# Kernel optimization log

Measured on AMD Instinct MI355X. Metric: run time of the kernel, lower is better.

The kernel has to match this reference:

```python
import jax, jax.numpy as jnp
import numpy as np

N, E, H, ED = 20000, 640000, 128, 16


def _lin_init(k, fan_in, fan_out):
    kw, kb = jax.random.split(k)
    lim = 1.0 / np.sqrt(fan_in)
    W = jax.random.uniform(kw, (fan_in, fan_out), jnp.float32, -lim, lim)
    b = jax.random.uniform(kb, (fan_out,), jnp.float32, -lim, lim)
    return W, b


def setup_inputs() -> dict:
    key = jax.random.key(0)
    ks = jax.random.split(key, 12)
    h = jax.random.normal(ks[0], (N, H), jnp.float32)
    x = jax.random.normal(ks[1], (N, 3), jnp.float32)
    edge_index = jax.random.randint(ks[2], (2, E), 0, N, jnp.int32)
    edge_attr = jax.random.normal(ks[3], (E, ED), jnp.float32)
    fixed_mask = jax.random.randint(ks[4], (N,), 0, 2, jnp.int32).astype(bool)
    We1, be1 = _lin_init(ks[5], 2 * H + 1 + ED, H)
    We2, be2 = _lin_init(ks[6], H, H)
    Wx1, bx1 = _lin_init(ks[7], H, H)
    Wx2, bx2 = _lin_init(ks[8], H, 1)
    Wh1, bh1 = _lin_init(ks[9], 2 * H, H)
    Wh2, bh2 = _lin_init(ks[10], H, H)
    return {"h": h, "x": x, "edge_index": edge_index, "edge_attr": edge_attr,
            "fixed_mask": fixed_mask,
            "We1": We1, "be1": be1, "We2": We2, "be2": be2,
            "Wx1": Wx1, "bx1": bx1, "Wx2": Wx2, "bx2": bx2,
            "Wh1": Wh1, "bh1": bh1, "Wh2": Wh2, "bh2": bh2}


def reference(h, x, edge_index, edge_attr, fixed_mask,
              We1, be1, We2, be2, Wx1, bx1, Wx2, bx2, Wh1, bh1, Wh2, bh2):
    src, dst = edge_index[0], edge_index[1]
    n = h.shape[0]
    diff = x[src] - x[dst]                               # [E,3]
    dist_sq_norm = jnp.sum(diff * diff, -1, keepdims=True) / 100.0
    e_in = jnp.concatenate([h[src], h[dst], dist_sq_norm, edge_attr], -1)
    m_ij = jax.nn.silu(jax.nn.silu(e_in @ We1 + be1) @ We2 + be2)  # [E,H]
    coord_w = jnp.tanh(jax.nn.silu(m_ij @ Wx1 + bx1) @ Wx2 + bx2)  # [E,1]
    coord_agg = jax.ops.segment_sum(diff * coord_w, dst, num_segments=n)
    coord_agg = coord_agg * (~fixed_mask).astype(h.dtype)[:, None]
    msg_agg = jax.ops.segment_sum(m_ij, dst, num_segments=n)       # [N,H]
    h_new = h + jax.nn.silu(jnp.concatenate([h, msg_agg], -1) @ Wh1 + bh1) @ Wh2 + bh2
    x_new = x + coord_agg
    return h_new, x_new
```

## Files before the change

### kernel.cpp

```cpp
#include <hip/hip_runtime.h>
#include <hip/hip_bf16.h>
#include <math.h>

#define NN   20000
#define NE   640000
#define HD   128
#define EDIM 16
#define KIN  273
#define P2   136

#define S_PWT   4096
#define S_PWE1M 32768
#define S_PW4   16384
#define S_PWH1  32768
#define S_PWH2  16384

typedef __bf16 bf16x8 __attribute__((ext_vector_type(8)));
typedef float  f32x4  __attribute__((ext_vector_type(4)));

__device__ __forceinline__ float silu_f(float v) {
    const float e = __expf(-v);
    return v * __builtin_amdgcn_rcpf(1.0f + e);
}
__device__ __forceinline__ float tanh_f(float s) {
    const float e = __expf(2.0f * s);
    return 1.0f - 2.0f * __builtin_amdgcn_rcpf(e + 1.0f);
}
__device__ __forceinline__ unsigned short f2bf(float f) {
    __bf16 b = (__bf16)f;
    return __builtin_bit_cast(unsigned short, b);
}
__device__ __forceinline__ float bf2f(unsigned short u) {
    __bf16 b = __builtin_bit_cast(__bf16, u);
    return (float)b;
}
__device__ __forceinline__ unsigned pack2bf(float a, float b) {
    return (unsigned)f2bf(a) | ((unsigned)f2bf(b) << 16);
}

__device__ __forceinline__ void pack_id(const float* __restrict__ W, int Kreal,
                                        unsigned short* __restrict__ P, int idx) {
    const int f = idx >> 9, r = idx & 511;
    const int lane = r >> 3, j = r & 7;
    const int kb = f >> 3, nb = f & 7;
    const int k = kb * 32 + (lane >> 4) * 8 + j;
    const int n = nb * 16 + (lane & 15);
    P[idx] = f2bf((k < Kreal) ? W[(size_t)k * HD + n] : 0.0f);
}
__device__ __forceinline__ void pack_il(const float* __restrict__ W, int Kreal,
                                        unsigned short* __restrict__ P, int idx) {
    const int f = idx >> 9, r = idx & 511;
    const int lane = r >> 3, j = r & 7;
    const int kb = f >> 3, nb = f & 7;
    const int k = kb * 32 + (lane >> 4) * 8 + j;
    const int n = (nb >> 1) * 32 + 2 * (lane & 15) + (nb & 1);
    P[idx] = f2bf((k < Kreal) ? W[(size_t)k * HD + n] : 0.0f);
}

__global__ void egnn_prep_kernel(
    const float* __restrict__ h, const int* __restrict__ ei,
    const float* __restrict__ We1, const float* __restrict__ We2,
    const float* __restrict__ Wx1, const float* __restrict__ Wh1,
    const float* __restrict__ Wh2,
    unsigned short* __restrict__ hb,
    unsigned short* __restrict__ PWt,  unsigned short* __restrict__ PWe1m,
    unsigned short* __restrict__ PWe2, unsigned short* __restrict__ PWx1,
    unsigned short* __restrict__ PWh1, unsigned short* __restrict__ PWh2,
    int* __restrict__ cnt)
{
    const size_t NH = (size_t)NN * HD;
    const size_t T1 = NH + S_PWT, T2 = T1 + S_PWE1M, T3 = T2 + S_PW4;
    const size_t T4 = T3 + S_PW4, T5 = T4 + S_PWH1, T6 = T5 + S_PWH2;
    const size_t TOT = T6 + NE;
    const size_t stride = (size_t)gridDim.x * blockDim.x;
    for (size_t i = (size_t)blockIdx.x * blockDim.x + threadIdx.x; i < TOT; i += stride) {
        if (i < NH) { hb[i] = f2bf(h[i]); continue; }
        if (i < T1) {
            const int idx = (int)(i - NH);
            const int r = idx & 511, nb = idx >> 9;
            const int lane = r >> 3, j = r & 7;
            const int k = 256 + (lane >> 4) * 8 + j;
            const int n = (nb >> 1) * 32 + 2 * (lane & 15) + (nb & 1);
            PWt[idx] = f2bf((k < KIN) ? We1[(size_t)k * HD + n] : 0.0f);
            continue;
        }
        if (i < T2) { pack_il(We1, 256, PWe1m, (int)(i - T1)); continue; }
        if (i < T3) { pack_il(We2, HD, PWe2, (int)(i - T2)); continue; }
        if (i < T4) { pack_il(Wx1, HD, PWx1, (int)(i - T3)); continue; }
        if (i < T5) { pack_id(Wh1, 2 * HD, PWh1, (int)(i - T4)); continue; }
        if (i < T6) { pack_id(Wh2, HD, PWh2, (int)(i - T5)); continue; }
        atomicAdd(&cnt[ei[NE + (i - T6)]], 1);
    }
}

__global__ __launch_bounds__(256, 4) void egnn_pre_kernel(
    const unsigned short* __restrict__ hb,
    const unsigned short* __restrict__ PWe1m, const float* __restrict__ be1,
    const int* __restrict__ cnt, int* __restrict__ cursor,
    unsigned short* __restrict__ preS, unsigned short* __restrict__ preD)
{
    const int t = threadIdx.x;
    if (blockIdx.x == 313) {
        __shared__ int ls[256];
        const int base = t * 79;
        int c[79];
        int s = 0;
        for (int i = 0; i < 79; ++i) {
            const int idx = base + i;
            c[i] = (idx < NN) ? cnt[idx] : 0;
            s += c[i];
        }
        ls[t] = s;
        __syncthreads();
        int v = s;
        for (int off = 1; off < 256; off <<= 1) {
            const int u = (t >= off) ? ls[t - off] : 0;
            __syncthreads();
            v += u;
            ls[t] = v;
            __syncthreads();
        }
        int run = v - s;
        for (int i = 0; i < 79; ++i) {
            const int idx = base + i;
            if (idx < NN) { cursor[idx] = run; run += c[i]; }
        }
        return;
    }
    const int n0 = blockIdx.x * 64;
    const int lane = t & 63, w = t >> 6;
    const int quad = lane >> 4, l16 = lane & 15;
    int arow[4];
    #pragma unroll
    for (int mb = 0; mb < 4; ++mb) arow[mb] = min(n0 + mb * 16 + l16, NN - 1);

    f32x4 accS[4][2], accD[4][2];
    #pragma unroll
    for (int mb = 0; mb < 4; ++mb)
        #pragma unroll
        for (int nt = 0; nt < 2; ++nt) {
            accS[mb][nt] = (f32x4){0.f,0.f,0.f,0.f};
            accD[mb][nt] = (f32x4){0.f,0.f,0.f,0.f};
        }
    #pragma unroll
    for (int kb = 0; kb < 4; ++kb) {
        bf16x8 a[4], bS[2], bD[2];
        #pragma unroll
        for (int mb = 0; mb < 4; ++mb)
            a[mb] = *(const bf16x8*)&hb[(size_t)arow[mb] * HD + kb * 32 + quad * 8];
        #pragma unroll
        for (int nt = 0; nt < 2; ++nt) {
            bS[nt] = *(const bf16x8*)&PWe1m[((kb * 8 + w * 2 + nt) * 64 + lane) * 8];
            bD[nt] = *(const bf16x8*)&PWe1m[(((4 + kb) * 8 + w * 2 + nt) * 64 + lane) * 8];
        }
        #pragma unroll
        for (int mb = 0; mb < 4; ++mb)
            #pragma unroll
            for (int nt = 0; nt < 2; ++nt) {
                accS[mb][nt] = __builtin_amdgcn_mfma_f32_16x16x32_bf16(
                    a[mb], bS[nt], accS[mb][nt], 0, 0, 0);
                accD[mb][nt] = __builtin_amdgcn_mfma_f32_16x16x32_bf16(
                    a[mb], bD[nt], accD[mb][nt], 0, 0, 0);
            }
    }
    const int cb = w * 32 + 2 * l16;
    const float2 b1 = *(const float2*)&be1[cb];
    #pragma unroll
    for (int mb = 0; mb < 4; ++mb)
        #pragma unroll
        for (int r = 0; r < 4; ++r) {
            const int n = n0 + mb * 16 + quad * 4 + r;
            if (n < NN) {
                *(unsigned*)&preS[(size_t)n * HD + cb] =
                    pack2bf(accS[mb][0][r], accS[mb][1][r]);
                *(unsigned*)&preD[(size_t)n * HD + cb] =
                    pack2bf(accD[mb][0][r] + b1.x, accD[mb][1][r] + b1.y);
            }
        }
}

__global__ void egnn_perm_kernel(const int* __restrict__ ei,
                                 int* __restrict__ cursor, int* __restrict__ perm) {
    const int e = blockIdx.x * 256 + threadIdx.x;
    const int pos = atomicAdd(&cursor[ei[NE + e]], 1);
    perm[pos] = e;
}

__global__ __launch_bounds__(256, 4) void egnn_edge_kernel(
    const unsigned short* __restrict__ preS, const unsigned short* __restrict__ preD,
    const float* __restrict__ x,
    const int* __restrict__ ei, const float* __restrict__ eattr,
    const int* __restrict__ perm,
    const unsigned short* __restrict__ PWt,
    const unsigned short* __restrict__ PWe2, const float* __restrict__ be2,
    const unsigned short* __restrict__ PWx1, const float* __restrict__ bx1,
    const float* __restrict__ Wx2, const float* __restrict__ bx2,
    float* __restrict__ msg_agg, float* __restrict__ coord_agg)
{
    __shared__ __align__(16) unsigned short tail[64 * 32];
    __shared__ __align__(16) unsigned short sT[64 * P2];
    __shared__ __align__(16) unsigned short sM[64 * P2];
    __shared__ int   sE[64], sSrc[64], sDst[64];
    __shared__ float sDiff[64][3];
    __shared__ float sW[64];

    const int t  = threadIdx.x;
    const int e0 = blockIdx.x * 64;

    if (t < 64) {
        const int e = perm[e0 + t];
        sE[t] = e;
        const int s = ei[e];
        const int d = ei[NE + e];
        sSrc[t] = s; sDst[t] = d;
        const float dx = x[s*3+0] - x[d*3+0];
        const float dy = x[s*3+1] - x[d*3+1];
        const float dz = x[s*3+2] - x[d*3+2];
        sDiff[t][0] = dx; sDiff[t][1] = dy; sDiff[t][2] = dz;
        tail[t * 32 + 0] = f2bf((dx*dx + dy*dy + dz*dz) * 0.01f);
    }
    __syncthreads();

    const int lane = t & 63;
    const int w    = t >> 6;
    const int quad = lane >> 4;
    const int l16  = lane & 15;
    const int cb   = w * 32 + 2 * l16;

    f32x4 preC[4][2];
    #pragma unroll
    for (int mb = 0; mb < 4; ++mb)
        #pragma unroll
        for (int r = 0; r < 4; ++r) {
            const int row = mb * 16 + quad * 4 + r;
            const unsigned us = *(const unsigned*)&preS[(size_t)sSrc[row] * HD + cb];
            const unsigned ud = *(const unsigned*)&preD[(size_t)sDst[row] * HD + cb];
            preC[mb][0][r] = bf2f((unsigned short)(us & 0xffff)) +
                             bf2f((unsigned short)(ud & 0xffff));
            preC[mb][1][r] = bf2f((unsigned short)(us >> 16)) +
                             bf2f((unsigned short)(ud >> 16));
        }

    {
        const int eL = t >> 2, q = t & 3;
        const int eG = sE[eL];
        #pragma unroll
        for (int jj = 0; jj < 8; ++jj) {
            const int col = q * 8 + jj;
            if (col == 0) continue;
            float v = 0.0f;
            if (col <= EDIM) v = eattr[(size_t)eG * EDIM + (col - 1)];
            tail[eL * 32 + col] = f2bf(v);
        }
    }
    __syncthreads();

    f32x4 acc1[4][2];
    {
        bf16x8 a[4], b[2];
        #pragma unroll
        for (int mb = 0; mb < 4; ++mb)
            a[mb] = *(const bf16x8*)&tail[(mb * 16 + l16) * 32 + quad * 8];
        #pragma unroll
        for (int nt = 0; nt < 2; ++nt)
            b[nt] = *(const bf16x8*)&PWt[((w * 2 + nt) * 64 + lane) * 8];
        #pragma unroll
        for (int mb = 0; mb < 4; ++mb)
            #pragma unroll
            for (int nt = 0; nt < 2; ++nt)
                acc1[mb][nt] = __builtin_amdgcn_mfma_f32_16x16x32_bf16(
                    a[mb], b[nt], preC[mb][nt], 0, 0, 0);
    }
    #pragma unroll
    for (int mb = 0; mb < 4; ++mb)
        #pragma unroll
        for (int r = 0; r < 4; ++r) {
            const int row = mb * 16 + quad * 4 + r;
            *(unsigned*)&sT[row * P2 + cb] =
                pack2bf(silu_f(acc1[mb][0][r]), silu_f(acc1[mb][1][r]));
        }
    __syncthreads();

    f32x4 acc2[4][2];
    #pragma unroll
    for (int mb = 0; mb < 4; ++mb)
        #pragma unroll
        for (int nt = 0; nt < 2; ++nt) acc2[mb][nt] = (f32x4){0.f,0.f,0.f,0.f};
    #pragma unroll
    for (int kb = 0; kb < 4; ++kb) {
        bf16x8 a[4], b[2];
        #pragma unroll
        for (int mb = 0; mb < 4; ++mb)
            a[mb] = *(const bf16x8*)&sT[(mb * 16 + l16) * P2 + kb * 32 + quad * 8];
        #pragma unroll
        for (int nt = 0; nt < 2; ++nt)
            b[nt] = *(const bf16x8*)&PWe2[((kb * 8 + w * 2 + nt) * 64 + lane) * 8];
        #pragma unroll
        for (int mb = 0; mb < 4; ++mb)
            #pragma unroll
            for (int nt = 0; nt < 2; ++nt)
                acc2[mb][nt] = __builtin_amdgcn_mfma_f32_16x16x32_bf16(
                    a[mb], b[nt], acc2[mb][nt], 0, 0, 0);
    }
    {
        const float2 b2 = *(const float2*)&be2[cb];
        #pragma unroll
        for (int mb = 0; mb < 4; ++mb)
            #pragma unroll
            for (int r = 0; r < 4; ++r) {
                const int row = mb * 16 + quad * 4 + r;
                *(unsigned*)&sM[row * P2 + cb] =
                    pack2bf(silu_f(acc2[mb][0][r] + b2.x),
                            silu_f(acc2[mb][1][r] + b2.y));
            }
    }
    __syncthreads();

    {
        const int ch   = t & 127;
        const int half = t >> 7;
        const int r0   = half * 32;
        float acc = 0.0f;
        #pragma unroll 4
        for (int r = 0; r < 32; ++r) {
            const int row = r0 + r;
            const int d   = sDst[row];
            acc += bf2f(sM[row * P2 + ch]);
            const bool flush = (r == 31) || (sDst[row + 1] != d);
            if (flush) {
                atomicAdd(&msg_agg[(size_t)d * HD + ch], acc);
                acc = 0.0f;
            }
        }
    }

    f32x4 acc3[4][2];
    #pragma unroll
    for (int mb = 0; mb < 4; ++mb)
        #pragma unroll
        for (int nt = 0; nt < 2; ++nt) acc3[mb][nt] = (f32x4){0.f,0.f,0.f,0.f};
    #pragma unroll
    for (int kb = 0; kb < 4; ++kb) {
        bf16x8 a[4], b[2];
        #pragma unroll
        for (int mb = 0; mb < 4; ++mb)
            a[mb] = *(const bf16x8*)&sM[(mb * 16 + l16) * P2 + kb * 32 + quad * 8];
        #pragma unroll
        for (int nt = 0; nt < 2; ++nt)
            b[nt] = *(const bf16x8*)&PWx1[((kb * 8 + w * 2 + nt) * 64 + lane) * 8];
        #pragma unroll
        for (int mb = 0; mb < 4; ++mb)
            #pragma unroll
            for (int nt = 0; nt < 2; ++nt)
                acc3[mb][nt] = __builtin_amdgcn_mfma_f32_16x16x32_bf16(
                    a[mb], b[nt], acc3[mb][nt], 0, 0, 0);
    }
    {
        const float2 bx = *(const float2*)&bx1[cb];
        const float2 w2 = *(const float2*)&Wx2[cb];
        float p[4][4];
        #pragma unroll
        for (int mb = 0; mb < 4; ++mb)
            #pragma unroll
            for (int r = 0; r < 4; ++r)
                p[mb][r] = silu_f(acc3[mb][0][r] + bx.x) * w2.x +
                           silu_f(acc3[mb][1][r] + bx.y) * w2.y;
        #pragma unroll
        for (int off = 8; off >= 1; off >>= 1)
            #pragma unroll
            for (int mb = 0; mb < 4; ++mb)
                #pragma unroll
                for (int r = 0; r < 4; ++r)
                    p[mb][r] += __shfl_xor(p[mb][r], off, 64);
        if (l16 == 0) {
            float* red = reinterpret_cast<float*>(sT);
            #pragma unroll
            for (int mb = 0; mb < 4; ++mb)
                #pragma unroll
                for (int r = 0; r < 4; ++r)
                    red[w * 64 + mb * 16 + quad * 4 + r] = p[mb][r];
        }
    }
    __syncthreads();
    if (t < 64) {
        const float* red = reinterpret_cast<const float*>(sT);
        sW[t] = tanh_f(red[t] + red[64 + t] + red[128 + t] + red[192 + t] + bx2[0]);
    }
    __syncthreads();

    if (w < 3) {
        const int dstv = sDst[lane];
        float v = sDiff[lane][w] * sW[lane];
        #pragma unroll
        for (int off = 1; off <= 32; off <<= 1) {
            const int   dn = __shfl_down(dstv, off, 64);
            const float vn = __shfl_down(v, off, 64);
            if (lane + off < 64 && dn == dstv) v += vn;
        }
        const int up = __shfl_up(dstv, 1, 64);
        if (lane == 0 || up != dstv)
            atomicAdd(&coord_agg[(size_t)dstv * 3 + w], v);
    }
}

__global__ __launch_bounds__(256, 4) void egnn_node_kernel(
    const unsigned short* __restrict__ hb, const float* __restrict__ h,
    const float* __restrict__ x, const int* __restrict__ fixed_mask,
    const unsigned short* __restrict__ PWh1, const float* __restrict__ bh1,
    const unsigned short* __restrict__ PWh2, const float* __restrict__ bh2,
    const float* __restrict__ msg_agg, const float* __restrict__ coord_agg,
    float* __restrict__ out_h, float* __restrict__ out_x)
{
    __shared__ __align__(16) unsigned short sTn[64 * P2];
    const int t  = threadIdx.x;
    const int n0 = blockIdx.x * 64;
    const int lane = t & 63, w = t >> 6;
    const int quad = lane >> 4, l16 = lane & 15;

    if (t < 192) {
        const int ln = t / 3, d3 = t - ln * 3;
        const int n  = n0 + ln;
        if (n < NN) {
            const float add = (fixed_mask[n] != 0) ? 0.0f : coord_agg[(size_t)n*3 + d3];
            out_x[(size_t)n*3 + d3] = x[(size_t)n*3 + d3] + add;
        }
    }

    int nrow[4];
    #pragma unroll
    for (int mb = 0; mb < 4; ++mb) nrow[mb] = min(n0 + mb * 16 + l16, NN - 1);

    f32x4 acc[4][2];
    #pragma unroll
    for (int mb = 0; mb < 4; ++mb)
        #pragma unroll
        for (int nt = 0; nt < 2; ++nt) acc[mb][nt] = (f32x4){0.f,0.f,0.f,0.f};

    #pragma unroll
    for (int kb = 0; kb < 8; ++kb) {
        bf16x8 a[4], b[2];
        if (kb < 4) {
            #pragma unroll
            for (int mb = 0; mb < 4; ++mb)
                a[mb] = *(const bf16x8*)&hb[(size_t)nrow[mb] * HD + kb * 32 + quad * 8];
        } else {
            #pragma unroll
            for (int mb = 0; mb < 4; ++mb) {
                const float* mp = msg_agg + (size_t)nrow[mb] * HD + (kb - 4) * 32 + quad * 8;
                const float4 v0 = ((const float4*)mp)[0];
                const float4 v1 = ((const float4*)mp)[1];
                bf16x8 av;
                av[0]=(__bf16)v0.x; av[1]=(__bf16)v0.y; av[2]=(__bf16)v0.z; av[3]=(__bf16)v0.w;
                av[4]=(__bf16)v1.x; av[5]=(__bf16)v1.y; av[6]=(__bf16)v1.z; av[7]=(__bf16)v1.w;
                a[mb] = av;
            }
        }
        #pragma unroll
        for (int nt = 0; nt < 2; ++nt)
            b[nt] = *(const bf16x8*)&PWh1[((kb * 8 + w * 2 + nt) * 64 + lane) * 8];
        #pragma unroll
        for (int mb = 0; mb < 4; ++mb)
            #pragma unroll
            for (int nt = 0; nt < 2; ++nt)
                acc[mb][nt] = __builtin_amdgcn_mfma_f32_16x16x32_bf16(
                    a[mb], b[nt], acc[mb][nt], 0, 0, 0);
    }
    #pragma unroll
    for (int nt = 0; nt < 2; ++nt) {
        const int col = w * 32 + nt * 16 + l16;
        const float bias = bh1[col];
        #pragma unroll
        for (int mb = 0; mb < 4; ++mb)
            #pragma unroll
            for (int r = 0; r < 4; ++r) {
                const int row = mb * 16 + quad * 4 + r;
                sTn[row * P2 + col] = f2bf(silu_f(acc[mb][nt][r] + bias));
            }
    }
    __syncthreads();

    #pragma unroll
    for (int mb = 0; mb < 4; ++mb)
        #pragma unroll
        for (int nt = 0; nt < 2; ++nt) acc[mb][nt] = (f32x4){0.f,0.f,0.f,0.f};
    #pragma unroll
    for (int kb = 0; kb < 4; ++kb) {
        bf16x8 a[4], b[2];
        #pragma unroll
        for (int mb = 0; mb < 4; ++mb)
            a[mb] = *(const bf16x8*)&sTn[(mb * 16 + l16) * P2 + kb * 32 + quad * 8];
        #pragma unroll
        for (int nt = 0; nt < 2; ++nt)
            b[nt] = *(const bf16x8*)&PWh2[((kb * 8 + w * 2 + nt) * 64 + lane) * 8];
        #pragma unroll
        for (int mb = 0; mb < 4; ++mb)
            #pragma unroll
            for (int nt = 0; nt < 2; ++nt)
                acc[mb][nt] = __builtin_amdgcn_mfma_f32_16x16x32_bf16(
                    a[mb], b[nt], acc[mb][nt], 0, 0, 0);
    }
    #pragma unroll
    for (int nt = 0; nt < 2; ++nt) {
        const int col = w * 32 + nt * 16 + l16;
        const float bias = bh2[col];
        #pragma unroll
        for (int mb = 0; mb < 4; ++mb)
            #pragma unroll
            for (int r = 0; r < 4; ++r) {
                const int row = mb * 16 + quad * 4 + r;
                const int n   = n0 + row;
                if (n < NN)
                    out_h[(size_t)n * HD + col] =
                        h[(size_t)n * HD + col] + acc[mb][nt][r] + bias;
            }
    }
}

extern "C" void kernel_launch(void* const* d_in, const int* in_sizes, int n_in,
                              void* d_out, int out_size, void* d_ws, size_t ws_size,
                              hipStream_t stream)
{
    const float* h     = (const float*)d_in[0];
    const float* x     = (const float*)d_in[1];
    const int*   ei    = (const int*)d_in[2];
    const float* eattr = (const float*)d_in[3];
    const int*   fmask = (const int*)d_in[4];
    const float* We1   = (const float*)d_in[5];
    const float* be1   = (const float*)d_in[6];
    const float* We2   = (const float*)d_in[7];
    const float* be2   = (const float*)d_in[8];
    const float* Wx1   = (const float*)d_in[9];
    const float* bx1   = (const float*)d_in[10];
    const float* Wx2   = (const float*)d_in[11];
    const float* bx2   = (const float*)d_in[12];
    const float* Wh1   = (const float*)d_in[13];
    const float* bh1   = (const float*)d_in[14];
    const float* Wh2   = (const float*)d_in[15];
    const float* bh2   = (const float*)d_in[16];

    float* msg    = (float*)d_ws;
    float* coord  = msg + (size_t)NN * HD;
    int*   cnt    = (int*)(coord + (size_t)NN * 3);
    int*   cursor = cnt + NN;
    int*   perm   = cursor + NN;
    unsigned short* hb    = (unsigned short*)(perm + NE);
    unsigned short* preS  = hb + (size_t)NN * HD;
    unsigned short* preD  = preS + (size_t)NN * HD;
    unsigned short* PWt   = preD + (size_t)NN * HD;
    unsigned short* PWe1m = PWt + S_PWT;
    unsigned short* PWe2  = PWe1m + S_PWE1M;
    unsigned short* PWx1  = PWe2 + S_PW4;
    unsigned short* PWh1  = PWx1 + S_PW4;
    unsigned short* PWh2  = PWh1 + S_PWH1;

    float* out_h = (float*)d_out;
    float* out_x = out_h + (size_t)NN * HD;

    hipMemsetAsync(d_ws, 0, (size_t)NN * (HD + 3 + 1) * sizeof(float), stream);
    egnn_prep_kernel<<<1024, 256, 0, stream>>>(
        h, ei, We1, We2, Wx1, Wh1, Wh2,
        hb, PWt, PWe1m, PWe2, PWx1, PWh1, PWh2, cnt);
    egnn_pre_kernel<<<314, 256, 0, stream>>>(hb, PWe1m, be1, cnt, cursor, preS, preD);
    egnn_perm_kernel<<<NE / 256, 256, 0, stream>>>(ei, cursor, perm);
    egnn_edge_kernel<<<NE / 64, 256, 0, stream>>>(
        preS, preD, x, ei, eattr, perm, PWt, PWe2, be2, PWx1, bx1,
        Wx2, bx2, msg, coord);
    egnn_node_kernel<<<(NN + 63) / 64, 256, 0, stream>>>(
        hb, h, x, fmask, PWh1, bh1, PWh2, bh2, msg, coord, out_h, out_x);
}
```

Before: 396.4 us.

## Merge memset, prep, pre-GEMM and permutation build into one cooperative kernel

```diff
diff --git a/kernel.cpp b/kernel.cpp
--- a/kernel.cpp
+++ b/kernel.cpp
@@ -1,6 +1,9 @@
 #include <hip/hip_runtime.h>
 #include <hip/hip_bf16.h>
+#include <hip/hip_cooperative_groups.h>
 #include <math.h>
+
+namespace cg = cooperative_groups;
 
 #define NN   20000
 #define NE   640000
@@ -14,6 +17,11 @@
 #define S_PW4   16384
 #define S_PWH1  32768
 #define S_PWH2  16384
+#define WPACK   (S_PWT + S_PWE1M + 2*S_PW4 + S_PWH1 + S_PWH2)
+
+#define COOPB   512
+#define ZDW     (NN*HD + NN*3 + NN)
+#define HCAST4  (NN*HD/4)
 
 typedef __bf16 bf16x8 __attribute__((ext_vector_type(8)));
 typedef float  f32x4  __attribute__((ext_vector_type(4)));
@@ -57,57 +65,127 @@
     P[idx] = f2bf((k < Kreal) ? W[(size_t)k * HD + n] : 0.0f);
 }
 
-__global__ void egnn_prep_kernel(
+__global__ __launch_bounds__(256, 2) void egnn_coop_kernel(
     const float* __restrict__ h, const int* __restrict__ ei,
     const float* __restrict__ We1, const float* __restrict__ We2,
     const float* __restrict__ Wx1, const float* __restrict__ Wh1,
-    const float* __restrict__ Wh2,
+    const float* __restrict__ Wh2, const float* __restrict__ be1,
+    int* __restrict__ zbase,
     unsigned short* __restrict__ hb,
     unsigned short* __restrict__ PWt,  unsigned short* __restrict__ PWe1m,
     unsigned short* __restrict__ PWe2, unsigned short* __restrict__ PWx1,
     unsigned short* __restrict__ PWh1, unsigned short* __restrict__ PWh2,
-    int* __restrict__ cnt)
+    unsigned short* __restrict__ preS, unsigned short* __restrict__ preD,
+    int* __restrict__ cnt, int* __restrict__ cursor, int* __restrict__ perm)
 {
-    const size_t NH = (size_t)NN * HD;
-    const size_t T1 = NH + S_PWT, T2 = T1 + S_PWE1M, T3 = T2 + S_PW4;
-    const size_t T4 = T3 + S_PW4, T5 = T4 + S_PWH1, T6 = T5 + S_PWH2;
-    const size_t TOT = T6 + NE;
-    const size_t stride = (size_t)gridDim.x * blockDim.x;
-    for (size_t i = (size_t)blockIdx.x * blockDim.x + threadIdx.x; i < TOT; i += stride) {
-        if (i < NH) { hb[i] = f2bf(h[i]); continue; }
-        if (i < T1) {
-            const int idx = (int)(i - NH);
-            const int r = idx & 511, nb = idx >> 9;
-            const int lane = r >> 3, j = r & 7;
-            const int k = 256 + (lane >> 4) * 8 + j;
-            const int n = (nb >> 1) * 32 + 2 * (lane & 15) + (nb & 1);
-            PWt[idx] = f2bf((k < KIN) ? We1[(size_t)k * HD + n] : 0.0f);
-            continue;
-        }
-        if (i < T2) { pack_il(We1, 256, PWe1m, (int)(i - T1)); continue; }
-        if (i < T3) { pack_il(We2, HD, PWe2, (int)(i - T2)); continue; }
-        if (i < T4) { pack_il(Wx1, HD, PWx1, (int)(i - T3)); continue; }
-        if (i < T5) { pack_id(Wh1, 2 * HD, PWh1, (int)(i - T4)); continue; }
-        if (i < T6) { pack_id(Wh2, HD, PWh2, (int)(i - T5)); continue; }
-        atomicAdd(&cnt[ei[NE + (i - T6)]], 1);
-    }
-}
-
-__global__ __launch_bounds__(256, 4) void egnn_pre_kernel(
-    const unsigned short* __restrict__ hb,
-    const unsigned short* __restrict__ PWe1m, const float* __restrict__ be1,
-    const int* __restrict__ cnt, int* __restrict__ cursor,
-    unsigned short* __restrict__ preS, unsigned short* __restrict__ preD)
-{
+    cg::grid_group grid = cg::this_grid();
     const int t = threadIdx.x;
-    if (blockIdx.x == 313) {
+    const int b = blockIdx.x;
+    const int gid = b * 256 + t;
+    const int gstride = COOPB * 256;
+
+    {
+        const int TOT = ZDW + HCAST4 + WPACK;
+        for (int i = gid; i < TOT; i += gstride) {
+            if (i < ZDW) { zbase[i] = 0; continue; }
+            int r = i - ZDW;
+            if (r < HCAST4) {
+                const float4 v = ((const float4*)h)[r];
+                unsigned* dst = (unsigned*)&hb[(size_t)r * 4];
+                dst[0] = pack2bf(v.x, v.y);
+                dst[1] = pack2bf(v.z, v.w);
+                continue;
+            }
+            r -= HCAST4;
+            if (r < S_PWT) {
+                const int rr = r & 511, nb = r >> 9;
+                const int lane = rr >> 3, j = rr & 7;
+                const int k = 256 + (lane >> 4) * 8 + j;
+                const int n = (nb >> 1) * 32 + 2 * (lane & 15) + (nb & 1);
+                PWt[r] = f2bf((k < KIN) ? We1[(size_t)k * HD + n] : 0.0f);
+                continue;
+            }
+            r -= S_PWT;
+            if (r < S_PWE1M) { pack_il(We1, 256, PWe1m, r); continue; }
+            r -= S_PWE1M;
+            if (r < S_PW4) { pack_il(We2, HD, PWe2, r); continue; }
+            r -= S_PW4;
+            if (r < S_PW4) { pack_il(Wx1, HD, PWx1, r); continue; }
+            r -= S_PW4;
+            if (r < S_PWH1) { pack_id(Wh1, 2 * HD, PWh1, r); continue; }
+            r -= S_PWH1;
+            pack_id(Wh2, HD, PWh2, r);
+        }
+    }
+    grid.sync();
+
+    if (b < 313) {
+        const int n0 = b * 64;
+        const int lane = t & 63, w = t >> 6;
+        const int quad = lane >> 4, l16 = lane & 15;
+        int arow[4];
+        #pragma unroll
+        for (int mb = 0; mb < 4; ++mb) arow[mb] = min(n0 + mb * 16 + l16, NN - 1);
+
+        f32x4 accS[4][2], accD[4][2];
+        #pragma unroll
+        for (int mb = 0; mb < 4; ++mb)
+            #pragma unroll
+            for (int nt = 0; nt < 2; ++nt) {
+                accS[mb][nt] = (f32x4){0.f,0.f,0.f,0.f};
+                accD[mb][nt] = (f32x4){0.f,0.f,0.f,0.f};
+            }
+        #pragma unroll
+        for (int kb = 0; kb < 4; ++kb) {
+            bf16x8 a[4], bS[2], bD[2];
+            #pragma unroll
+            for (int mb = 0; mb < 4; ++mb)
+                a[mb] = *(const bf16x8*)&hb[(size_t)arow[mb] * HD + kb * 32 + quad * 8];
+            #pragma unroll
+            for (int nt = 0; nt < 2; ++nt) {
+                bS[nt] = *(const bf16x8*)&PWe1m[((kb * 8 + w * 2 + nt) * 64 + lane) * 8];
+                bD[nt] = *(const bf16x8*)&PWe1m[(((4 + kb) * 8 + w * 2 + nt) * 64 + lane) * 8];
+            }
+            #pragma unroll
+            for (int mb = 0; mb < 4; ++mb)
+                #pragma unroll
+                for (int nt = 0; nt < 2; ++nt) {
+                    accS[mb][nt] = __builtin_amdgcn_mfma_f32_16x16x32_bf16(
+                        a[mb], bS[nt], accS[mb][nt], 0, 0, 0);
+                    accD[mb][nt] = __builtin_amdgcn_mfma_f32_16x16x32_bf16(
+                        a[mb], bD[nt], accD[mb][nt], 0, 0, 0);
+                }
+        }
+        const int cb = w * 32 + 2 * l16;
+        const float2 b1 = *(const float2*)&be1[cb];
+        #pragma unroll
+        for (int mb = 0; mb < 4; ++mb)
+            #pragma unroll
+            for (int r = 0; r < 4; ++r) {
+                const int n = n0 + mb * 16 + quad * 4 + r;
+                if (n < NN) {
+                    *(unsigned*)&preS[(size_t)n * HD + cb] =
+                        pack2bf(accS[mb][0][r], accS[mb][1][r]);
+                    *(unsigned*)&preD[(size_t)n * HD + cb] =
+                        pack2bf(accD[mb][0][r] + b1.x, accD[mb][1][r] + b1.y);
+                }
+            }
+    } else {
+        for (int e = (b - 313) * 256 + t; e < NE; e += (COOPB - 313) * 256)
+            atomicAdd(&cnt[ei[NE + e]], 1);
+    }
+    grid.sync();
+
+    if (b == 0) {
         __shared__ int ls[256];
         const int base = t * 79;
         int c[79];
         int s = 0;
         for (int i = 0; i < 79; ++i) {
             const int idx = base + i;
-            c[i] = (idx < NN) ? cnt[idx] : 0;
+            c[i] = (idx < NN)
+                 ? __hip_atomic_load(&cnt[idx], __ATOMIC_RELAXED, __HIP_MEMORY_SCOPE_AGENT)
+                 : 0;
             s += c[i];
         }
         ls[t] = s;
@@ -123,67 +201,19 @@
         int run = v - s;
         for (int i = 0; i < 79; ++i) {
             const int idx = base + i;
-            if (idx < NN) { cursor[idx] = run; run += c[i]; }
-        }
-        return;
-    }
-    const int n0 = blockIdx.x * 64;
-    const int lane = t & 63, w = t >> 6;
-    const int quad = lane >> 4, l16 = lane & 15;
-    int arow[4];
-    #pragma unroll
-    for (int mb = 0; mb < 4; ++mb) arow[mb] = min(n0 + mb * 16 + l16, NN - 1);
-
-    f32x4 accS[4][2], accD[4][2];
-    #pragma unroll
-    for (int mb = 0; mb < 4; ++mb)
-        #pragma unroll
-        for (int nt = 0; nt < 2; ++nt) {
-            accS[mb][nt] = (f32x4){0.f,0.f,0.f,0.f};
-            accD[mb][nt] = (f32x4){0.f,0.f,0.f,0.f};
-        }
-    #pragma unroll
-    for (int kb = 0; kb < 4; ++kb) {
-        bf16x8 a[4], bS[2], bD[2];
-        #pragma unroll
-        for (int mb = 0; mb < 4; ++mb)
-            a[mb] = *(const bf16x8*)&hb[(size_t)arow[mb] * HD + kb * 32 + quad * 8];
-        #pragma unroll
-        for (int nt = 0; nt < 2; ++nt) {
-            bS[nt] = *(const bf16x8*)&PWe1m[((kb * 8 + w * 2 + nt) * 64 + lane) * 8];
-            bD[nt] = *(const bf16x8*)&PWe1m[(((4 + kb) * 8 + w * 2 + nt) * 64 + lane) * 8];
-        }
-        #pragma unroll
-        for (int mb = 0; mb < 4; ++mb)
-            #pragma unroll
-            for (int nt = 0; nt < 2; ++nt) {
-                accS[mb][nt] = __builtin_amdgcn_mfma_f32_16x16x32_bf16(
-                    a[mb], bS[nt], accS[mb][nt], 0, 0, 0);
-                accD[mb][nt] = __builtin_amdgcn_mfma_f32_16x16x32_bf16(
-                    a[mb], bD[nt], accD[mb][nt], 0, 0, 0);
-            }
-    }
-    const int cb = w * 32 + 2 * l16;
-    const float2 b1 = *(const float2*)&be1[cb];
-    #pragma unroll
-    for (int mb = 0; mb < 4; ++mb)
-        #pragma unroll
-        for (int r = 0; r < 4; ++r) {
-            const int n = n0 + mb * 16 + quad * 4 + r;
-            if (n < NN) {
-                *(unsigned*)&preS[(size_t)n * HD + cb] =
-                    pack2bf(accS[mb][0][r], accS[mb][1][r]);
-                *(unsigned*)&preD[(size_t)n * HD + cb] =
-                    pack2bf(accD[mb][0][r] + b1.x, accD[mb][1][r] + b1.y);
-            }
-        }
-}
-
-__global__ void egnn_perm_kernel(const int* __restrict__ ei,
-                                 int* __restrict__ cursor, int* __restrict__ perm) {
-    const int e = blockIdx.x * 256 + threadIdx.x;
-    const int pos = atomicAdd(&cursor[ei[NE + e]], 1);
-    perm[pos] = e;
+            if (idx < NN) {
+                __hip_atomic_store(&cursor[idx], run, __ATOMIC_RELAXED,
+                                   __HIP_MEMORY_SCOPE_AGENT);
+                run += c[i];
+            }
+        }
+    }
+    grid.sync();
+
+    for (int e = gid; e < NE; e += gstride) {
+        const int pos = atomicAdd(&cursor[ei[NE + e]], 1);
+        perm[pos] = e;
+    }
 }
 
 __global__ __launch_bounds__(256, 4) void egnn_edge_kernel(
@@ -556,12 +586,16 @@
     float* out_h = (float*)d_out;
     float* out_x = out_h + (size_t)NN * HD;
 
-    hipMemsetAsync(d_ws, 0, (size_t)NN * (HD + 3 + 1) * sizeof(float), stream);
-    egnn_prep_kernel<<<1024, 256, 0, stream>>>(
-        h, ei, We1, We2, Wx1, Wh1, Wh2,
-        hb, PWt, PWe1m, PWe2, PWx1, PWh1, PWh2, cnt);
-    egnn_pre_kernel<<<314, 256, 0, stream>>>(hb, PWe1m, be1, cnt, cursor, preS, preD);
-    egnn_perm_kernel<<<NE / 256, 256, 0, stream>>>(ei, cursor, perm);
+    int* zbase = (int*)d_ws;
+    void* cargs[] = {
+        (void*)&h, (void*)&ei, (void*)&We1, (void*)&We2, (void*)&Wx1,
+        (void*)&Wh1, (void*)&Wh2, (void*)&be1, (void*)&zbase, (void*)&hb,
+        (void*)&PWt, (void*)&PWe1m, (void*)&PWe2, (void*)&PWx1, (void*)&PWh1,
+        (void*)&PWh2, (void*)&preS, (void*)&preD, (void*)&cnt, (void*)&cursor,
+        (void*)&perm
+    };
+    hipLaunchCooperativeKernel((void*)egnn_coop_kernel, dim3(COOPB), dim3(256),
+                               cargs, 0, stream);
     egnn_edge_kernel<<<NE / 64, 256, 0, stream>>>(
         preS, preD, x, ei, eattr, perm, PWt, PWe2, be2, PWx1, bx1,
         Wx2, bx2, msg, coord);
```

After: 596.8 us. +50.6%, slower.

## Fuse perm build into pre kernel via grid flag; vectorize h cast and msg scatter

Applied to the files above, without the earlier changes.

```diff
diff --git a/kernel.cpp b/kernel.cpp
--- a/kernel.cpp
+++ b/kernel.cpp
@@ -14,6 +14,8 @@
 #define S_PW4   16384
 #define S_PWH1  32768
 #define S_PWH2  16384
+
+#define PREB    314
 
 typedef __bf16 bf16x8 __attribute__((ext_vector_type(8)));
 typedef float  f32x4  __attribute__((ext_vector_type(4)));
@@ -68,15 +70,21 @@
     unsigned short* __restrict__ PWh1, unsigned short* __restrict__ PWh2,
     int* __restrict__ cnt)
 {
-    const size_t NH = (size_t)NN * HD;
-    const size_t T1 = NH + S_PWT, T2 = T1 + S_PWE1M, T3 = T2 + S_PW4;
+    const size_t NH4 = (size_t)NN * HD / 4;
+    const size_t T1 = NH4 + S_PWT, T2 = T1 + S_PWE1M, T3 = T2 + S_PW4;
     const size_t T4 = T3 + S_PW4, T5 = T4 + S_PWH1, T6 = T5 + S_PWH2;
     const size_t TOT = T6 + NE;
     const size_t stride = (size_t)gridDim.x * blockDim.x;
     for (size_t i = (size_t)blockIdx.x * blockDim.x + threadIdx.x; i < TOT; i += stride) {
-        if (i < NH) { hb[i] = f2bf(h[i]); continue; }
+        if (i < NH4) {
+            const float4 v = ((const float4*)h)[i];
+            unsigned* dst = (unsigned*)&hb[(size_t)i * 4];
+            dst[0] = pack2bf(v.x, v.y);
+            dst[1] = pack2bf(v.z, v.w);
+            continue;
+        }
         if (i < T1) {
-            const int idx = (int)(i - NH);
+            const int idx = (int)(i - NH4);
             const int r = idx & 511, nb = idx >> 9;
             const int lane = r >> 3, j = r & 7;
             const int k = 256 + (lane >> 4) * 8 + j;
@@ -93,21 +101,26 @@
     }
 }
 
-__global__ __launch_bounds__(256, 4) void egnn_pre_kernel(
-    const unsigned short* __restrict__ hb,
+__global__ __launch_bounds__(256, 4) void egnn_preperm_kernel(
+    const unsigned short* __restrict__ hb, const int* __restrict__ ei,
     const unsigned short* __restrict__ PWe1m, const float* __restrict__ be1,
     const int* __restrict__ cnt, int* __restrict__ cursor,
+    int* __restrict__ flag, int* __restrict__ perm,
     unsigned short* __restrict__ preS, unsigned short* __restrict__ preD)
 {
     const int t = threadIdx.x;
-    if (blockIdx.x == 313) {
+    const int b = blockIdx.x;
+
+    if (b == 313) {
         __shared__ int ls[256];
         const int base = t * 79;
         int c[79];
         int s = 0;
         for (int i = 0; i < 79; ++i) {
             const int idx = base + i;
-            c[i] = (idx < NN) ? cnt[idx] : 0;
+            c[i] = (idx < NN)
+                 ? __hip_atomic_load(&cnt[idx], __ATOMIC_RELAXED, __HIP_MEMORY_SCOPE_AGENT)
+                 : 0;
             s += c[i];
         }
         ls[t] = s;
@@ -123,67 +136,80 @@
         int run = v - s;
         for (int i = 0; i < 79; ++i) {
             const int idx = base + i;
-            if (idx < NN) { cursor[idx] = run; run += c[i]; }
-        }
-        return;
-    }
-    const int n0 = blockIdx.x * 64;
-    const int lane = t & 63, w = t >> 6;
-    const int quad = lane >> 4, l16 = lane & 15;
-    int arow[4];
-    #pragma unroll
-    for (int mb = 0; mb < 4; ++mb) arow[mb] = min(n0 + mb * 16 + l16, NN - 1);
-
-    f32x4 accS[4][2], accD[4][2];
-    #pragma unroll
-    for (int mb = 0; mb < 4; ++mb)
-        #pragma unroll
-        for (int nt = 0; nt < 2; ++nt) {
-            accS[mb][nt] = (f32x4){0.f,0.f,0.f,0.f};
-            accD[mb][nt] = (f32x4){0.f,0.f,0.f,0.f};
-        }
-    #pragma unroll
-    for (int kb = 0; kb < 4; ++kb) {
-        bf16x8 a[4], bS[2], bD[2];
-        #pragma unroll
-        for (int mb = 0; mb < 4; ++mb)
-            a[mb] = *(const bf16x8*)&hb[(size_t)arow[mb] * HD + kb * 32 + quad * 8];
-        #pragma unroll
-        for (int nt = 0; nt < 2; ++nt) {
-            bS[nt] = *(const bf16x8*)&PWe1m[((kb * 8 + w * 2 + nt) * 64 + lane) * 8];
-            bD[nt] = *(const bf16x8*)&PWe1m[(((4 + kb) * 8 + w * 2 + nt) * 64 + lane) * 8];
-        }
+            if (idx < NN) {
+                __hip_atomic_store(&cursor[idx], run, __ATOMIC_RELAXED,
+                                   __HIP_MEMORY_SCOPE_AGENT);
+                run += c[i];
+            }
+        }
+        __syncthreads();
+        __threadfence();
+        if (t == 0)
+            __hip_atomic_store(flag, 1, __ATOMIC_RELEASE, __HIP_MEMORY_SCOPE_AGENT);
+    } else {
+        const int n0 = b * 64;
+        const int lane = t & 63, w = t >> 6;
+        const int quad = lane >> 4, l16 = lane & 15;
+        int arow[4];
+        #pragma unroll
+        for (int mb = 0; mb < 4; ++mb) arow[mb] = min(n0 + mb * 16 + l16, NN - 1);
+
+        f32x4 accS[4][2], accD[4][2];
         #pragma unroll
         for (int mb = 0; mb < 4; ++mb)
             #pragma unroll
             for (int nt = 0; nt < 2; ++nt) {
-                accS[mb][nt] = __builtin_amdgcn_mfma_f32_16x16x32_bf16(
-                    a[mb], bS[nt], accS[mb][nt], 0, 0, 0);
-                accD[mb][nt] = __builtin_amdgcn_mfma_f32_16x16x32_bf16(
-                    a[mb], bD[nt], accD[mb][nt], 0, 0, 0);
-            }
-    }
-    const int cb = w * 32 + 2 * l16;
-    const float2 b1 = *(const float2*)&be1[cb];
-    #pragma unroll
-    for (int mb = 0; mb < 4; ++mb)
-        #pragma unroll
-        for (int r = 0; r < 4; ++r) {
-            const int n = n0 + mb * 16 + quad * 4 + r;
-            if (n < NN) {
-                *(unsigned*)&preS[(size_t)n * HD + cb] =
-                    pack2bf(accS[mb][0][r], accS[mb][1][r]);
-                *(unsigned*)&preD[(size_t)n * HD + cb] =
-                    pack2bf(accD[mb][0][r] + b1.x, accD[mb][1][r] + b1.y);
-            }
-        }
-}
-
-__global__ void egnn_perm_kernel(const int* __restrict__ ei,
-                                 int* __restrict__ cursor, int* __restrict__ perm) {
-    const int e = blockIdx.x * 256 + threadIdx.x;
-    const int pos = atomicAdd(&cursor[ei[NE + e]], 1);
-    perm[pos] = e;
+                accS[mb][nt] = (f32x4){0.f,0.f,0.f,0.f};
+                accD[mb][nt] = (f32x4){0.f,0.f,0.f,0.f};
+            }
+        #pragma unroll
+        for (int kb = 0; kb < 4; ++kb) {
+            bf16x8 a[4], bS[2], bD[2];
+            #pragma unroll
+            for (int mb = 0; mb < 4; ++mb)
+                a[mb] = *(const bf16x8*)&hb[(size_t)arow[mb] * HD + kb * 32 + quad * 8];
+            #pragma unroll
+            for (int nt = 0; nt < 2; ++nt) {
+                bS[nt] = *(const bf16x8*)&PWe1m[((kb * 8 + w * 2 + nt) * 64 + lane) * 8];
+                bD[nt] = *(const bf16x8*)&PWe1m[(((4 + kb) * 8 + w * 2 + nt) * 64 + lane) * 8];
+            }
+            #pragma unroll
+            for (int mb = 0; mb < 4; ++mb)
+                #pragma unroll
+                for (int nt = 0; nt < 2; ++nt) {
+                    accS[mb][nt] = __builtin_amdgcn_mfma_f32_16x16x32_bf16(
+                        a[mb], bS[nt], accS[mb][nt], 0, 0, 0);
+                    accD[mb][nt] = __builtin_amdgcn_mfma_f32_16x16x32_bf16(
+                        a[mb], bD[nt], accD[mb][nt], 0, 0, 0);
+                }
+        }
+        const int cb = w * 32 + 2 * l16;
+        const float2 b1 = *(const float2*)&be1[cb];
+        #pragma unroll
+        for (int mb = 0; mb < 4; ++mb)
+            #pragma unroll
+            for (int r = 0; r < 4; ++r) {
+                const int n = n0 + mb * 16 + quad * 4 + r;
+                if (n < NN) {
+                    *(unsigned*)&preS[(size_t)n * HD + cb] =
+                        pack2bf(accS[mb][0][r], accS[mb][1][r]);
+                    *(unsigned*)&preD[(size_t)n * HD + cb] =
+                        pack2bf(accD[mb][0][r] + b1.x, accD[mb][1][r] + b1.y);
+                }
+            }
+    }
+
+    if (t == 0) {
+        while (__hip_atomic_load(flag, __ATOMIC_ACQUIRE, __HIP_MEMORY_SCOPE_AGENT) == 0)
+            __builtin_amdgcn_s_sleep(8);
+    }
+    __syncthreads();
+    const int gid = b * 256 + t;
+    const int gstride = PREB * 256;
+    for (int e = gid; e < NE; e += gstride) {
+        const int pos = atomicAdd(&cursor[ei[NE + e]], 1);
+        perm[pos] = e;
+    }
 }
 
 __global__ __launch_bounds__(256, 4) void egnn_edge_kernel(
@@ -317,19 +343,21 @@
     __syncthreads();
 
     {
-        const int ch   = t & 127;
-        const int half = t >> 7;
-        const int r0   = half * 32;
-        float acc = 0.0f;
+        const int cp = t & 63;
+        const int r0 = (t >> 6) * 16;
+        float a0 = 0.0f, a1 = 0.0f;
         #pragma unroll 4
-        for (int r = 0; r < 32; ++r) {
+        for (int r = 0; r < 16; ++r) {
             const int row = r0 + r;
             const int d   = sDst[row];
-            acc += bf2f(sM[row * P2 + ch]);
-            const bool flush = (r == 31) || (sDst[row + 1] != d);
+            const unsigned u = *(const unsigned*)&sM[row * P2 + 2 * cp];
+            a0 += bf2f((unsigned short)(u & 0xffff));
+            a1 += bf2f((unsigned short)(u >> 16));
+            const bool flush = (r == 15) || (sDst[row + 1] != d);
             if (flush) {
-                atomicAdd(&msg_agg[(size_t)d * HD + ch], acc);
-                acc = 0.0f;
+                atomicAdd(&msg_agg[(size_t)d * HD + 2 * cp], a0);
+                atomicAdd(&msg_agg[(size_t)d * HD + 2 * cp + 1], a1);
+                a0 = 0.0f; a1 = 0.0f;
             }
         }
     }
@@ -541,7 +569,8 @@
     float* msg    = (float*)d_ws;
     float* coord  = msg + (size_t)NN * HD;
     int*   cnt    = (int*)(coord + (size_t)NN * 3);
-    int*   cursor = cnt + NN;
+    int*   flag   = cnt + NN;
+    int*   cursor = flag + 4;
     int*   perm   = cursor + NN;
     unsigned short* hb    = (unsigned short*)(perm + NE);
     unsigned short* preS  = hb + (size_t)NN * HD;
@@ -556,12 +585,12 @@
     float* out_h = (float*)d_out;
     float* out_x = out_h + (size_t)NN * HD;
 
-    hipMemsetAsync(d_ws, 0, (size_t)NN * (HD + 3 + 1) * sizeof(float), stream);
+    hipMemsetAsync(d_ws, 0, ((size_t)NN * (HD + 4) + 4) * sizeof(float), stream);
     egnn_prep_kernel<<<1024, 256, 0, stream>>>(
         h, ei, We1, We2, Wx1, Wh1, Wh2,
         hb, PWt, PWe1m, PWe2, PWx1, PWh1, PWh2, cnt);
-    egnn_pre_kernel<<<314, 256, 0, stream>>>(hb, PWe1m, be1, cnt, cursor, preS, preD);
-    egnn_perm_kernel<<<NE / 256, 256, 0, stream>>>(ei, cursor, perm);
+    egnn_preperm_kernel<<<PREB, 256, 0, stream>>>(
+        hb, ei, PWe1m, be1, cnt, cursor, flag, perm, preS, preD);
     egnn_edge_kernel<<<NE / 64, 256, 0, stream>>>(
         preS, preD, x, ei, eattr, perm, PWt, PWe2, be2, PWx1, bx1,
         Wx2, bx2, msg, coord);
```

Result: slower. 755.5 us (+90.6%).
